# Kernel tuning notes

Hardware: AMD Instinct MI355X
Metric: run time of the kernel (lower is better)

The kernel has to match this reference:

```python
import jax, jax.numpy as jnp
import numpy as np

NUM_CLASSES = 21
TOP_K = 200
CONF_THRESH = 0.01
NMS_THRESH = 0.45
VAR0, VAR1 = 0.1, 0.2
B, P = 64, 8732  # SSD300 VOC prior count


def setup_inputs() -> dict:
    key = jax.random.key(0)
    k1, k2, k3 = jax.random.split(key, 3)
    loc = jax.random.normal(k1, (B, P, 4), dtype=jnp.float32)
    conf = jax.random.normal(k2, (B, P, NUM_CLASSES), dtype=jnp.float32)
    priors = jax.random.uniform(k3, (P, 4), dtype=jnp.float32, minval=0.02, maxval=1.0)
    return {"loc": loc, "conf": conf, "priors": priors}


def _decode(loc, priors):
    # loc, priors: [P, 4] (cx, cy, w, h) offsets -> corner boxes [P, 4]
    cxcy = priors[:, :2] + loc[:, :2] * VAR0 * priors[:, 2:]
    wh = priors[:, 2:] * jnp.exp(loc[:, 2:] * VAR1)
    x1y1 = cxcy - wh * 0.5
    x2y2 = x1y1 + wh
    return jnp.concatenate([x1y1, x2y2], axis=1)


def _iou_matrix(boxes):
    # boxes [K,4] -> pairwise IoU [K,K] with the original +1 pixel convention
    x1, y1, x2, y2 = boxes[:, 0], boxes[:, 1], boxes[:, 2], boxes[:, 3]
    area = (x2 - x1 + 1.0) * (y2 - y1 + 1.0)
    xx1 = jnp.maximum(x1[:, None], x1[None, :])
    yy1 = jnp.maximum(y1[:, None], y1[None, :])
    xx2 = jnp.minimum(x2[:, None], x2[None, :])
    yy2 = jnp.minimum(y2[:, None], y2[None, :])
    w = jnp.maximum(0.0, xx2 - xx1 + 1.0)
    h = jnp.maximum(0.0, yy2 - yy1 + 1.0)
    inter = w * h
    return inter / (area[:, None] + area[None, :] - inter)


def _nms_keep(boxes, valid):
    # boxes [K,4] sorted by descending score; greedy NMS as a fixed-length loop
    K = boxes.shape[0]
    iou = _iou_matrix(boxes)
    later = jnp.arange(K)[None, :] > jnp.arange(K)[:, None]  # strictly lower-priority

    def body(i, suppressed):
        keep_i = valid[i] & ~suppressed[i]
        return suppressed | (keep_i & (iou[i] > NMS_THRESH) & later[i])

    suppressed = jax.lax.fori_loop(0, K, body, jnp.zeros((K,), bool))
    return valid & ~suppressed


def _per_class(scores, decoded):
    # scores [P], decoded [P,4] -> [TOP_K, 7] rows (score, x1, y1, x2, y2, 0, 0)
    valid_p = scores > CONF_THRESH
    s = jnp.where(valid_p, scores, -1.0)
    top_s, idx = jax.lax.top_k(s, TOP_K)
    b = decoded[idx]                      # [K,4]
    valid = top_s > CONF_THRESH
    keep = _nms_keep(b, valid)
    rows = jnp.concatenate([top_s[:, None], b], axis=1)  # [K,5]
    order = jnp.argsort(~keep)            # stable: kept rows compacted to front
    rows = jnp.where(keep[order][:, None], rows[order], 0.0)
    return jnp.pad(rows, ((0, 0), (0, 2)))  # pad to width 7 (original leaves cols 5:7 zero)


def _per_image(loc_i, conf_i, priors):
    decoded = _decode(loc_i, priors)      # [P,4]
    # classes 1..C-1 (skip background class 0)
    cls_scores = conf_i[:, 1:].T          # [C-1, P]
    cls_out = jax.vmap(lambda s: _per_class(s, decoded))(cls_scores)  # [C-1,K,7]
    bg = jnp.zeros((1, TOP_K, 7), dtype=loc_i.dtype)
    return jnp.concatenate([bg, cls_out], axis=0)  # [C,K,7]


def _detect(loc, conf, priors):
    conf_soft = jax.nn.softmax(conf, axis=-1)  # SSD test phase applies softmax
    output = jax.vmap(_per_image, in_axes=(0, 0, None))(loc, conf_soft, priors)  # [B,C,K,7]
    flt = output.reshape(output.shape[0], -1, 7)  # [B, C*K, 7]
    score = flt[:, :, 0]
    idx = jnp.argsort(-score, axis=1)
    rank = jnp.argsort(idx, axis=1)
    mask = rank < TOP_K
    order = jnp.argsort(~mask, axis=1)    # stable: top-K rows, original positional order
    sel = jnp.take_along_axis(flt, order[:, :TOP_K, None], axis=1)  # [B,K,7]
    return sel.reshape(-1, 7)             # [B*K, 7], matching flt[rank < top_k]


def reference(loc, conf, priors):
    return _detect(loc, conf, priors)
```

## Files before the change

kernel.cpp:

```cpp
#include <hip/hip_runtime.h>
#include <stdint.h>

#define NUM_P 8732
#define NUM_B 64
#define NUM_CLS 21
#define TOPK 200
#define NMS_T 0.45f
#define CONF_T 0.01f
#define NL 35
#define NV4 2183
#define NL2 16
#define MAXCAND 4000
#define ORD_SENT 0x407FFFFFu
#define HI_BITS 0x17800u

__device__ __forceinline__ uint32_t ordf(float f) {
    uint32_t u = __float_as_uint(f);
    return (u & 0x80000000u) ? ~u : (u | 0x80000000u);
}
__device__ __forceinline__ float unordf(uint32_t v) {
    uint32_t u = (v & 0x80000000u) ? (v ^ 0x80000000u) : ~v;
    return __uint_as_float(u);
}

__global__ __launch_bounds__(256) void prep_kernel(const float* __restrict__ conf,
                                                   uint32_t* __restrict__ ct,
                                                   uint32_t* __restrict__ candCount) {
    __shared__ float tile[256 * NUM_CLS];
    const int bx = blockIdx.x;
    const int b = blockIdx.y;
    const int tid = threadIdx.x;
    if (bx == 0 && b == 0 && tid < NUM_B) candCount[tid] = 0u;
    const int p0 = bx * 256;
    const int np = min(256, NUM_P - p0);
    const int nf4 = (np * NUM_CLS) / 4;
    const float4* src = reinterpret_cast<const float4*>(conf + ((size_t)b * NUM_P + p0) * NUM_CLS);
    float4* dst = reinterpret_cast<float4*>(tile);
#pragma unroll
    for (int i = 0; i < 6; ++i) {
        int idx = tid + i * 256;
        if (idx < nf4) dst[idx] = src[idx];
    }
    __syncthreads();
    if (tid < np) {
        const int p = p0 + tid;
        const float* row = tile + tid * NUM_CLS;
        float x[NUM_CLS];
#pragma unroll
        for (int c = 0; c < NUM_CLS; ++c) x[c] = row[c];
        float m = x[0];
#pragma unroll
        for (int c = 1; c < NUM_CLS; ++c) m = fmaxf(m, x[c]);
        float e[NUM_CLS];
        float s = 0.0f;
#pragma unroll
        for (int c = 0; c < NUM_CLS; ++c) { e[c] = expf(x[c] - m); s += e[c]; }
#pragma unroll
        for (int c = 1; c < NUM_CLS; ++c) {
            float sc = e[c] / s;
            float sv = (sc > CONF_T) ? sc : -1.0f;
            ct[((size_t)(b * 20 + (c - 1))) * NUM_P + p] = ordf(sv);
        }
    }
}

__global__ __launch_bounds__(256, 5) void select_nms_kernel(const uint32_t* __restrict__ ct,
                                                            const float* __restrict__ loc,
                                                            const float* __restrict__ priors,
                                                            float* __restrict__ selS,
                                                            float* __restrict__ selX1,
                                                            float* __restrict__ selY1,
                                                            float* __restrict__ selX2,
                                                            float* __restrict__ selY2,
                                                            uint64_t* __restrict__ cands,
                                                            uint32_t* __restrict__ candCount) {
    __shared__ uint32_t hist[2048];
    __shared__ uint64_t skey[256];
    __shared__ uint32_t wtot[4];
    __shared__ uint32_t sh_d, sh_above, sh_bnd, sh_nsent;
    __shared__ int scnt;
    __shared__ int sh_run;

    const int blk = blockIdx.x;
    const int b = blk / 20;
    const int c = blk % 20;
    const int tid = threadIdx.x;
    const int lane = tid & 63;
    const int wv = tid >> 6;
    const uint32_t* col = ct + (size_t)blk * NUM_P;
    const uint4* colv = reinterpret_cast<const uint4*>(col);

#pragma unroll
    for (int i = 0; i < 8; ++i) hist[tid + i * 256] = 0;
    skey[tid] = 0;
    if (tid == 0) { scnt = 0; sh_run = 0; }
    __syncthreads();

    uint4 vv[9];
#pragma unroll
    for (int i = 0; i < 9; ++i) {
        int idx = tid + i * 256;
        vv[i] = make_uint4(ORD_SENT, ORD_SENT, ORD_SENT, ORD_SENT);
        if (idx < NV4) vv[i] = colv[idx];
    }
    int nsent = 0;
#pragma unroll
    for (int i = 0; i < 9; ++i) {
        int idx = tid + i * 256;
        if (idx < NV4) {
            uint32_t a0 = vv[i].x, a1 = vv[i].y, a2 = vv[i].z, a3 = vv[i].w;
            if (a0 == ORD_SENT) nsent++; else atomicAdd(&hist[(a0 >> 15) & 2047u], 1u);
            if (a1 == ORD_SENT) nsent++; else atomicAdd(&hist[(a1 >> 15) & 2047u], 1u);
            if (a2 == ORD_SENT) nsent++; else atomicAdd(&hist[(a2 >> 15) & 2047u], 1u);
            if (a3 == ORD_SENT) nsent++; else atomicAdd(&hist[(a3 >> 15) & 2047u], 1u);
        }
    }
    {
        int v = nsent;
#pragma unroll
        for (int off = 32; off; off >>= 1) v += __shfl_down(v, off);
        if (lane == 0) wtot[wv] = (uint32_t)v;
        __syncthreads();
        if (tid == 0) sh_nsent = wtot[0] + wtot[1] + wtot[2] + wtot[3];
        __syncthreads();
    }
    const int nreal = NUM_P - (int)sh_nsent;

    uint32_t emitThr = 0;
    bool ranked = false;
    uint32_t thrEq = 0;
    int needEq = 0;

    if (nreal >= TOPK) {
        {
            const int tbase = tid * 8;
            uint32_t ls = 0;
#pragma unroll
            for (int j = 0; j < 8; ++j) ls += hist[tbase + j];
            uint32_t v = ls;
#pragma unroll
            for (int off = 1; off < 64; off <<= 1) {
                uint32_t o2 = __shfl_down(v, off);
                if (lane + off < 64) v += o2;
            }
            if (lane == 0) wtot[wv] = v;
            __syncthreads();
            uint32_t above_wave = 0;
            for (int w = wv + 1; w < 4; ++w) above_wave += wtot[w];
            uint32_t acc = (v + above_wave) - ls;
            for (int j = 7; j >= 0; --j) {
                uint32_t h = hist[tbase + j];
                if (acc < (uint32_t)TOPK && acc + h >= (uint32_t)TOPK) {
                    sh_d = (uint32_t)(tbase + j);
                    sh_above = acc;
                    sh_bnd = h;
                }
                acc += h;
            }
            __syncthreads();
        }
        uint32_t d1 = sh_d;
        int cert = (int)sh_above;
        int need = TOPK - cert;
        int bnd = (int)sh_bnd;
        const uint32_t lvl1 = HI_BITS | d1;

        if (cert + bnd <= 256) {
            emitThr = lvl1 << 15;
        } else {
            __syncthreads();
#pragma unroll
            for (int i = 0; i < 8; ++i) hist[tid + i * 256] = 0;
            __syncthreads();
#pragma unroll
            for (int i = 0; i < 9; ++i) {
                int idx = tid + i * 256;
                if (idx < NV4) {
                    if ((vv[i].x >> 15) == lvl1) atomicAdd(&hist[(vv[i].x >> 4) & 2047u], 1u);
                    if ((vv[i].y >> 15) == lvl1) atomicAdd(&hist[(vv[i].y >> 4) & 2047u], 1u);
                    if ((vv[i].z >> 15) == lvl1) atomicAdd(&hist[(vv[i].z >> 4) & 2047u], 1u);
                    if ((vv[i].w >> 15) == lvl1) atomicAdd(&hist[(vv[i].w >> 4) & 2047u], 1u);
                }
            }
            __syncthreads();
            {
                const int tbase = tid * 8;
                uint32_t ls = 0;
#pragma unroll
                for (int j = 0; j < 8; ++j) ls += hist[tbase + j];
                uint32_t v = ls;
#pragma unroll
                for (int off = 1; off < 64; off <<= 1) {
                    uint32_t o2 = __shfl_down(v, off);
                    if (lane + off < 64) v += o2;
                }
                if (lane == 0) wtot[wv] = v;
                __syncthreads();
                uint32_t above_wave = 0;
                for (int w = wv + 1; w < 4; ++w) above_wave += wtot[w];
                uint32_t acc = (v + above_wave) - ls;
                for (int j = 7; j >= 0; --j) {
                    uint32_t h = hist[tbase + j];
                    if (acc < (uint32_t)need && acc + h >= (uint32_t)need) {
                        sh_d = (uint32_t)(tbase + j);
                        sh_above = acc;
                        sh_bnd = h;
                    }
                    acc += h;
                }
                __syncthreads();
            }
            uint32_t d2 = sh_d;
            cert += (int)sh_above;
            need -= (int)sh_above;
            bnd = (int)sh_bnd;
            const uint32_t pfx28 = (lvl1 << 11) | d2;

            if (cert + bnd <= 256) {
                emitThr = pfx28 << 4;
            } else {
                __syncthreads();
                if (tid < 16) hist[tid] = 0;
                __syncthreads();
#pragma unroll
                for (int i = 0; i < 9; ++i) {
                    int idx = tid + i * 256;
                    if (idx < NV4) {
                        if ((vv[i].x >> 4) == pfx28) atomicAdd(&hist[vv[i].x & 15u], 1u);
                        if ((vv[i].y >> 4) == pfx28) atomicAdd(&hist[vv[i].y & 15u], 1u);
                        if ((vv[i].z >> 4) == pfx28) atomicAdd(&hist[vv[i].z & 15u], 1u);
                        if ((vv[i].w >> 4) == pfx28) atomicAdd(&hist[vv[i].w & 15u], 1u);
                    }
                }
                __syncthreads();
                if (tid == 0) {
                    uint32_t acc = 0;
                    for (int j = 15; j >= 0; --j) {
                        uint32_t h = hist[j];
                        if (acc < (uint32_t)need && acc + h >= (uint32_t)need) {
                            sh_d = (uint32_t)j; sh_above = acc; sh_bnd = h; break;
                        }
                        acc += h;
                    }
                }
                __syncthreads();
                uint32_t d3 = sh_d;
                cert += (int)sh_above;
                need -= (int)sh_above;
                bnd = (int)sh_bnd;
                const uint32_t pfx32 = (pfx28 << 4) | d3;
                if (cert + bnd <= 256) {
                    emitThr = pfx32;
                } else {
                    ranked = true; thrEq = pfx32; needEq = need;
                }
            }
        }
    } else {
        ranked = true; thrEq = ORD_SENT; needEq = TOPK - nreal;
    }

    if (!ranked) {
#pragma unroll
        for (int i = 0; i < 9; ++i) {
            int idx = tid + i * 256;
            if (idx < NV4) {
                uint32_t aa[4] = {vv[i].x, vv[i].y, vv[i].z, vv[i].w};
#pragma unroll
                for (int j = 0; j < 4; ++j) {
                    uint32_t o = aa[j];
                    if (o >= emitThr) {
                        int s0 = atomicAdd(&scnt, 1);
                        uint32_t p = (uint32_t)(idx * 4 + j);
                        if (s0 < 256)
                            skey[s0] = ((uint64_t)o << 32) | (0xFFFFFFFFu - p);
                    }
                }
            }
        }
        __syncthreads();
    } else {
        for (int i = 0; i < NL; ++i) {
            int p = i * 256 + tid;
            uint32_t o = (p < NUM_P) ? col[p] : 0u;
            if (o > thrEq) {
                int s0 = atomicAdd(&scnt, 1);
                if (s0 < 256)
                    skey[s0] = ((uint64_t)o << 32) | (0xFFFFFFFFu - (uint32_t)p);
            }
            bool tie = (p < NUM_P) && (o == thrEq);
            unsigned long long ball = __ballot(tie);
            if (lane == 0) wtot[wv] = (uint32_t)__popcll(ball);
            __syncthreads();
            int rank = sh_run;
            for (int w = 0; w < wv; ++w) rank += (int)wtot[w];
            rank += __popcll(ball & ((1ull << lane) - 1ull));
            if (tie && rank < needEq) {
                int s0 = atomicAdd(&scnt, 1);
                if (s0 < 256)
                    skey[s0] = ((uint64_t)o << 32) | (0xFFFFFFFFu - (uint32_t)p);
            }
            __syncthreads();
            if (tid == 0) sh_run += (int)(wtot[0] + wtot[1] + wtot[2] + wtot[3]);
            __syncthreads();
        }
    }

    uint64_t* skey2 = reinterpret_cast<uint64_t*>(hist + 1536);
    uint64_t myk = skey[tid];
    skey2[tid] = 0;
    __syncthreads();
    int rk = 0;
#pragma unroll 8
    for (int j = 0; j < 256; ++j) rk += (skey[j] > myk) ? 1 : 0;
    if (myk != 0) skey2[rk] = myk;
    __syncthreads();

    float4* bbox4 = reinterpret_cast<float4*>(hist);
    float*  dar   = reinterpret_cast<float*>(hist) + 4 * TOPK;
    float*  dsc   = reinterpret_cast<float*>(hist) + 5 * TOPK;
    uint64_t kreg = (tid < TOPK) ? skey2[tid] : 0;
    if (tid < TOPK) {
        uint32_t p = 0xFFFFFFFFu - (uint32_t)kreg;
        float msc = unordf((uint32_t)(kreg >> 32));
        const float4 l4 = reinterpret_cast<const float4*>(loc)[(size_t)b * NUM_P + p];
        const float4 pr = reinterpret_cast<const float4*>(priors)[p];
        float cx = pr.x + (l4.x * 0.1f) * pr.z;
        float cy = pr.y + (l4.y * 0.1f) * pr.w;
        float w  = pr.z * expf(l4.z * 0.2f);
        float h  = pr.w * expf(l4.w * 0.2f);
        float mx1 = cx - w * 0.5f;
        float my1 = cy - h * 0.5f;
        float mx2 = mx1 + w;
        float my2 = my1 + h;
        bbox4[tid] = make_float4(mx1, my1, mx2, my2);
        dar[tid] = (mx2 - mx1 + 1.0f) * (my2 - my1 + 1.0f);
        dsc[tid] = msc;
    }
    __syncthreads();
    if (wv != 0) return;

    float jx1[4], jy1[4], jx2[4], jy2[4], jar[4], jsc[4];
    uint64_t validb[4], supb[4];
#pragma unroll
    for (int s = 0; s < 4; ++s) {
        int idx = s * 64 + lane;
        bool v = idx < TOPK;
        float4 bx = v ? bbox4[idx] : make_float4(0.f, 0.f, 0.f, 0.f);
        jx1[s] = bx.x; jy1[s] = bx.y; jx2[s] = bx.z; jy2[s] = bx.w;
        jar[s] = v ? dar[idx] : 1.0f;
        jsc[s] = v ? dsc[idx] : -1.0f;
        validb[s] = __ballot(v && jsc[s] > CONF_T);
        supb[s] = 0;
    }

#pragma unroll
    for (int s = 0; s < 4; ++s) {
        const int nown = (s == 3) ? (TOPK - 3 * 64) : 64;
#pragma unroll 1
        for (int o = 0; o < nown; ++o) {
            if (((validb[s] & ~supb[s]) >> o) & 1ull) {
                const int i = s * 64 + o;
                const float4 bi = bbox4[i];
                const float iar = dar[i];
#pragma unroll
                for (int s2 = s; s2 < 4; ++s2) {
                    float xx1 = fmaxf(bi.x, jx1[s2]);
                    float yy1 = fmaxf(bi.y, jy1[s2]);
                    float xx2 = fminf(bi.z, jx2[s2]);
                    float yy2 = fminf(bi.w, jy2[s2]);
                    float w = fmaxf(0.0f, xx2 - xx1 + 1.0f);
                    float h = fmaxf(0.0f, yy2 - yy1 + 1.0f);
                    float inter = w * h;
                    float iou = inter / (iar + jar[s2] - inter);
                    int idx2 = s2 * 64 + lane;
                    bool later = (s2 > s) ? (idx2 < TOPK) : (lane > o);
                    bool hit = (iou > NMS_T) && later;
                    supb[s2] |= __ballot(hit);
                }
            }
        }
    }

    const size_t base = (size_t)blk * TOPK;
    int off = 0;
    uint64_t wkey[4];
    int wrank[4];
    bool wk[4];
#pragma unroll
    for (int s = 0; s < 4; ++s) {
        uint64_t ball = validb[s] & ~supb[s];
        bool kept = (ball >> lane) & 1ull;
        int rank = off + __popcll(ball & ((1ull << lane) - 1ull));
        wk[s] = kept;
        wrank[s] = rank;
        wkey[s] = 0;
        if (kept) {
            selS[base + rank] = jsc[s];
            selX1[base + rank] = jx1[s];
            selY1[base + rank] = jy1[s];
            selX2[base + rank] = jx2[s];
            selY2[base + rank] = jy2[s];
            uint32_t pos = (uint32_t)(c + 1) * TOPK + (uint32_t)rank;
            wkey[s] = ((uint64_t)ordf(jsc[s]) << 32) | (uint32_t)(0xFFFFFFFFu - pos);
        }
        off += __popcll(ball);
    }
    uint32_t bcast = 0;
    if (lane == 0) bcast = atomicAdd(&candCount[b], (uint32_t)off);
    bcast = (uint32_t)__shfl((int)bcast, 0);
#pragma unroll
    for (int s = 0; s < 4; ++s)
        if (wk[s]) cands[(size_t)b * MAXCAND + bcast + wrank[s]] = wkey[s];
}

__global__ __launch_bounds__(256) void final_kernel(const uint64_t* __restrict__ cands,
                                                    const uint32_t* __restrict__ candCount,
                                                    const float* __restrict__ selS,
                                                    const float* __restrict__ selX1,
                                                    const float* __restrict__ selY1,
                                                    const float* __restrict__ selX2,
                                                    const float* __restrict__ selY2,
                                                    float* __restrict__ out) {
    __shared__ uint32_t hist[2048];
    __shared__ uint64_t skey[256];
    __shared__ uint32_t posArr[TOPK];
    __shared__ uint32_t sortedPos[TOPK];
    __shared__ uint32_t wtot[4];
    __shared__ int wsum[2][4];
    __shared__ uint32_t sh_d, sh_above, sh_bnd;
    __shared__ int scnt;

    const int b = blockIdx.x;
    const int tid = threadIdx.x;
    const int lane = tid & 63;
    const int wv = tid >> 6;
    const int n = (int)candCount[b];

    uint64_t key[NL2];
#pragma unroll
    for (int i = 0; i < NL2; ++i) {
        int idx = tid + i * 256;
        key[i] = (idx < n) ? cands[(size_t)b * MAXCAND + idx] : 0ull;
    }
#pragma unroll
    for (int i = 0; i < 8; ++i) hist[tid + i * 256] = 0;
    skey[tid] = 0;
    if (tid == 0) scnt = 0;
    __syncthreads();

    uint64_t emitThr = 1;
    if (n > TOPK) {
#pragma unroll
        for (int i = 0; i < NL2; ++i)
            if (key[i] != 0ull) atomicAdd(&hist[(uint32_t)(key[i] >> 47) & 2047u], 1u);
        __syncthreads();
        {
            const int tbase = tid * 8;
            uint32_t ls = 0;
#pragma unroll
            for (int j = 0; j < 8; ++j) ls += hist[tbase + j];
            uint32_t v = ls;
#pragma unroll
            for (int off = 1; off < 64; off <<= 1) {
                uint32_t o2 = __shfl_down(v, off);
                if (lane + off < 64) v += o2;
            }
            if (lane == 0) wtot[wv] = v;
            __syncthreads();
            uint32_t above_wave = 0;
            for (int w = wv + 1; w < 4; ++w) above_wave += wtot[w];
            uint32_t acc = (v + above_wave) - ls;
            for (int j = 7; j >= 0; --j) {
                uint32_t h = hist[tbase + j];
                if (acc < (uint32_t)TOPK && acc + h >= (uint32_t)TOPK) {
                    sh_d = (uint32_t)(tbase + j);
                    sh_above = acc;
                    sh_bnd = h;
                }
                acc += h;
            }
            __syncthreads();
        }
        if (sh_above + sh_bnd <= 256u) {
            emitThr = (uint64_t)(HI_BITS | sh_d) << 47;
        } else {
            uint64_t prefix = 0;
            for (int bit = 63; bit >= 0; --bit) {
                uint64_t cand = prefix | (1ull << bit);
                int cnt = 0;
#pragma unroll
                for (int i = 0; i < NL2; ++i) cnt += (key[i] >= cand) ? 1 : 0;
                for (int off = 32; off; off >>= 1) cnt += __shfl_down(cnt, off);
                int bufi = bit & 1;
                if (lane == 0) wsum[bufi][wv] = cnt;
                __syncthreads();
                int tot = wsum[bufi][0] + wsum[bufi][1] + wsum[bufi][2] + wsum[bufi][3];
                if (tot >= TOPK) prefix = cand;
            }
            emitThr = prefix;
        }
    }

#pragma unroll
    for (int i = 0; i < NL2; ++i) {
        if (key[i] != 0ull && key[i] >= emitThr) {
            int s0 = atomicAdd(&scnt, 1);
            if (s0 < 256) skey[s0] = key[i];
        }
    }
    __syncthreads();
    const int nsel = min(scnt, TOPK);

    uint64_t myk = skey[tid];
    __syncthreads();
    int rk = 0;
#pragma unroll 8
    for (int j = 0; j < 256; ++j) rk += (skey[j] > myk) ? 1 : 0;
    if (myk != 0 && rk < TOPK) posArr[rk] = 0xFFFFFFFFu - (uint32_t)myk;
    __syncthreads();

    if (tid < nsel) {
        uint32_t mypos = posArr[tid];
        int pr = 0;
        for (int j = 0; j < nsel; ++j) pr += (posArr[j] < mypos) ? 1 : 0;
        sortedPos[pr] = mypos;
    }
    __syncthreads();

    if (tid < TOPK) {
        int T = TOPK - nsel;
        float* o = out + ((size_t)b * TOPK + tid) * 7;
        if (tid < T) {
            o[0] = 0.f; o[1] = 0.f; o[2] = 0.f; o[3] = 0.f; o[4] = 0.f; o[5] = 0.f; o[6] = 0.f;
        } else {
            uint32_t pos = sortedPos[tid - T];
            uint32_t cc = pos / TOPK;
            uint32_t sl = pos % TOPK;
            size_t r = ((size_t)b * 20 + (cc - 1)) * TOPK + sl;
            o[0] = selS[r]; o[1] = selX1[r]; o[2] = selY1[r]; o[3] = selX2[r]; o[4] = selY2[r];
            o[5] = 0.f; o[6] = 0.f;
        }
    }
}

extern "C" void kernel_launch(void* const* d_in, const int* in_sizes, int n_in,
                              void* d_out, int out_size, void* d_ws, size_t ws_size,
                              hipStream_t stream) {
    const float* loc    = (const float*)d_in[0];
    const float* conf   = (const float*)d_in[1];
    const float* priors = (const float*)d_in[2];
    float* out = (float*)d_out;

    const size_t CAND_BYTES = (size_t)NUM_B * MAXCAND * sizeof(uint64_t);
    const size_t SEL_ONE    = (size_t)NUM_B * 20 * TOPK * sizeof(float);
    const size_t CNT_BYTES  = 256;

    char* ws = (char*)d_ws;
    uint64_t* cands     = (uint64_t*)ws;
    float*    selS      = (float*)(ws + CAND_BYTES);
    float*    selX1     = (float*)(ws + CAND_BYTES + SEL_ONE);
    float*    selY1     = (float*)(ws + CAND_BYTES + 2 * SEL_ONE);
    float*    selX2     = (float*)(ws + CAND_BYTES + 3 * SEL_ONE);
    float*    selY2     = (float*)(ws + CAND_BYTES + 4 * SEL_ONE);
    uint32_t* candCount = (uint32_t*)(ws + CAND_BYTES + 5 * SEL_ONE);
    uint32_t* ct        = (uint32_t*)(ws + CAND_BYTES + 5 * SEL_ONE + CNT_BYTES);

    dim3 pgrid(35, NUM_B);
    prep_kernel<<<pgrid, 256, 0, stream>>>(conf, ct, candCount);
    select_nms_kernel<<<NUM_B * 20, 256, 0, stream>>>(ct, loc, priors,
                                                      selS, selX1, selY1, selX2, selY2,
                                                      cands, candCount);
    final_kernel<<<NUM_B, 256, 0, stream>>>(cands, candCount,
                                            selS, selX1, selY1, selX2, selY2, out);
}
```

Before: 63.73 us.

## Compress class-score columns to 16-bit keys and recompute exact scores for selected candidates

The prep kernel now writes a 16-bit truncated order-preserving key per prior and class, padded to an aligned pitch, plus the per-prior softmax max and sum, in place of full 32-bit keys. The select kernel builds its histograms on the 16-bit keys, keeps candidate prior indices, resolves ties at the threshold bucket by recomputing exact softmax scores from conf, and rebuilds the 64-bit sort keys only for the selected entries. This halves the intermediate score traffic and cuts the number of radix refinement passes. In exchange it adds a denominator buffer, scattered conf reloads for the selected candidates, and a more complex tie-handling path.

```diff
diff --git a/kernel.cpp b/kernel.cpp
--- a/kernel.cpp
+++ b/kernel.cpp
@@ -7,8 +7,8 @@
 #define TOPK 200
 #define NMS_T 0.45f
 #define CONF_T 0.01f
-#define NL 35
-#define NV4 2183
+#define PITCH16 8736
+#define NV8 1092
 #define NL2 16
 #define MAXCAND 4000
 #define ORD_SENT 0x407FFFFFu
@@ -24,7 +24,8 @@
 }
 
 __global__ __launch_bounds__(256) void prep_kernel(const float* __restrict__ conf,
-                                                   uint32_t* __restrict__ ct,
+                                                   uint16_t* __restrict__ ct16,
+                                                   float2* __restrict__ denom,
                                                    uint32_t* __restrict__ candCount) {
     __shared__ float tile[256 * NUM_CLS];
     const int bx = blockIdx.x;
@@ -55,16 +56,24 @@
         float s = 0.0f;
 #pragma unroll
         for (int c = 0; c < NUM_CLS; ++c) { e[c] = expf(x[c] - m); s += e[c]; }
+        denom[(size_t)b * NUM_P + p] = make_float2(m, s);
 #pragma unroll
         for (int c = 1; c < NUM_CLS; ++c) {
             float sc = e[c] / s;
-            float sv = (sc > CONF_T) ? sc : -1.0f;
-            ct[((size_t)(b * 20 + (c - 1))) * NUM_P + p] = ordf(sv);
-        }
+            uint16_t u = 0;
+            if (sc > CONF_T) u = (uint16_t)((ordf(sc) >> 10) & 0xFFFFu);
+            ct16[((size_t)(b * 20 + (c - 1))) * PITCH16 + p] = u;
+        }
+    } else if (p0 + tid >= NUM_P && p0 + tid < PITCH16) {
+#pragma unroll
+        for (int c = 1; c < NUM_CLS; ++c)
+            ct16[((size_t)(b * 20 + (c - 1))) * PITCH16 + (p0 + tid)] = 0;
     }
 }
 
-__global__ __launch_bounds__(256, 5) void select_nms_kernel(const uint32_t* __restrict__ ct,
+__global__ __launch_bounds__(256, 5) void select_nms_kernel(const uint16_t* __restrict__ ct16,
+                                                            const float* __restrict__ conf,
+                                                            const float2* __restrict__ denom,
                                                             const float* __restrict__ loc,
                                                             const float* __restrict__ priors,
                                                             float* __restrict__ selS,
@@ -76,8 +85,9 @@
                                                             uint32_t* __restrict__ candCount) {
     __shared__ uint32_t hist[2048];
     __shared__ uint64_t skey[256];
+    __shared__ uint32_t plist[256];
     __shared__ uint32_t wtot[4];
-    __shared__ uint32_t sh_d, sh_above, sh_bnd, sh_nsent;
+    __shared__ uint32_t sh_d, sh_above, sh_bnd, sh_nsent, sh_tcnt;
     __shared__ int scnt;
     __shared__ int sh_run;
 
@@ -87,32 +97,34 @@
     const int tid = threadIdx.x;
     const int lane = tid & 63;
     const int wv = tid >> 6;
-    const uint32_t* col = ct + (size_t)blk * NUM_P;
-    const uint4* colv = reinterpret_cast<const uint4*>(col);
+    const uint4* colv = reinterpret_cast<const uint4*>(ct16 + (size_t)blk * PITCH16);
+    const size_t ibase = (size_t)b * NUM_P;
 
 #pragma unroll
     for (int i = 0; i < 8; ++i) hist[tid + i * 256] = 0;
     skey[tid] = 0;
-    if (tid == 0) { scnt = 0; sh_run = 0; }
-    __syncthreads();
-
-    uint4 vv[9];
-#pragma unroll
-    for (int i = 0; i < 9; ++i) {
+    if (tid == 0) { scnt = 0; sh_run = 0; sh_tcnt = 0; }
+    __syncthreads();
+
+    uint4 uu[5];
+#pragma unroll
+    for (int i = 0; i < 5; ++i) {
         int idx = tid + i * 256;
-        vv[i] = make_uint4(ORD_SENT, ORD_SENT, ORD_SENT, ORD_SENT);
-        if (idx < NV4) vv[i] = colv[idx];
+        uu[i] = make_uint4(0, 0, 0, 0);
+        if (idx < NV8) uu[i] = colv[idx];
     }
     int nsent = 0;
 #pragma unroll
-    for (int i = 0; i < 9; ++i) {
+    for (int i = 0; i < 5; ++i) {
         int idx = tid + i * 256;
-        if (idx < NV4) {
-            uint32_t a0 = vv[i].x, a1 = vv[i].y, a2 = vv[i].z, a3 = vv[i].w;
-            if (a0 == ORD_SENT) nsent++; else atomicAdd(&hist[(a0 >> 15) & 2047u], 1u);
-            if (a1 == ORD_SENT) nsent++; else atomicAdd(&hist[(a1 >> 15) & 2047u], 1u);
-            if (a2 == ORD_SENT) nsent++; else atomicAdd(&hist[(a2 >> 15) & 2047u], 1u);
-            if (a3 == ORD_SENT) nsent++; else atomicAdd(&hist[(a3 >> 15) & 2047u], 1u);
+        if (idx < NV8) {
+            uint32_t ww[4] = {uu[i].x, uu[i].y, uu[i].z, uu[i].w};
+#pragma unroll
+            for (int q = 0; q < 4; ++q) {
+                uint32_t lo = ww[q] & 0xFFFFu, hi = ww[q] >> 16;
+                if (lo) atomicAdd(&hist[lo >> 5], 1u); else nsent++;
+                if (hi) atomicAdd(&hist[hi >> 5], 1u); else nsent++;
+            }
         }
     }
     {
@@ -124,12 +136,11 @@
         if (tid == 0) sh_nsent = wtot[0] + wtot[1] + wtot[2] + wtot[3];
         __syncthreads();
     }
-    const int nreal = NUM_P - (int)sh_nsent;
-
-    uint32_t emitThr = 0;
-    bool ranked = false;
-    uint32_t thrEq = 0;
-    int needEq = 0;
+    const int nreal = PITCH16 - (int)sh_nsent;
+
+    int mode;
+    uint32_t thr16 = 1;
+    int need3 = 0, needEq = 0;
 
     if (nreal >= TOPK) {
         {
@@ -161,150 +172,198 @@
         }
         uint32_t d1 = sh_d;
         int cert = (int)sh_above;
-        int need = TOPK - cert;
         int bnd = (int)sh_bnd;
-        const uint32_t lvl1 = HI_BITS | d1;
 
         if (cert + bnd <= 256) {
-            emitThr = lvl1 << 15;
+            thr16 = d1 << 5;
+            mode = 0;
         } else {
             __syncthreads();
-#pragma unroll
-            for (int i = 0; i < 8; ++i) hist[tid + i * 256] = 0;
-            __syncthreads();
-#pragma unroll
-            for (int i = 0; i < 9; ++i) {
+            if (tid < 32) hist[tid] = 0;
+            __syncthreads();
+#pragma unroll
+            for (int i = 0; i < 5; ++i) {
                 int idx = tid + i * 256;
-                if (idx < NV4) {
-                    if ((vv[i].x >> 15) == lvl1) atomicAdd(&hist[(vv[i].x >> 4) & 2047u], 1u);
-                    if ((vv[i].y >> 15) == lvl1) atomicAdd(&hist[(vv[i].y >> 4) & 2047u], 1u);
-                    if ((vv[i].z >> 15) == lvl1) atomicAdd(&hist[(vv[i].z >> 4) & 2047u], 1u);
-                    if ((vv[i].w >> 15) == lvl1) atomicAdd(&hist[(vv[i].w >> 4) & 2047u], 1u);
-                }
-            }
-            __syncthreads();
-            {
-                const int tbase = tid * 8;
-                uint32_t ls = 0;
-#pragma unroll
-                for (int j = 0; j < 8; ++j) ls += hist[tbase + j];
-                uint32_t v = ls;
-#pragma unroll
-                for (int off = 1; off < 64; off <<= 1) {
-                    uint32_t o2 = __shfl_down(v, off);
-                    if (lane + off < 64) v += o2;
-                }
-                if (lane == 0) wtot[wv] = v;
-                __syncthreads();
-                uint32_t above_wave = 0;
-                for (int w = wv + 1; w < 4; ++w) above_wave += wtot[w];
-                uint32_t acc = (v + above_wave) - ls;
-                for (int j = 7; j >= 0; --j) {
-                    uint32_t h = hist[tbase + j];
+                if (idx < NV8) {
+                    uint32_t ww[4] = {uu[i].x, uu[i].y, uu[i].z, uu[i].w};
+#pragma unroll
+                    for (int q = 0; q < 4; ++q) {
+                        uint32_t lo = ww[q] & 0xFFFFu, hi = ww[q] >> 16;
+                        if ((lo >> 5) == d1) atomicAdd(&hist[lo & 31u], 1u);
+                        if ((hi >> 5) == d1) atomicAdd(&hist[hi & 31u], 1u);
+                    }
+                }
+            }
+            __syncthreads();
+            const int need = TOPK - cert;
+            if (tid == 0) {
+                uint32_t acc = 0;
+                for (int j = 31; j >= 0; --j) {
+                    uint32_t h = hist[j];
                     if (acc < (uint32_t)need && acc + h >= (uint32_t)need) {
-                        sh_d = (uint32_t)(tbase + j);
-                        sh_above = acc;
-                        sh_bnd = h;
+                        sh_d = (uint32_t)j; sh_above = acc; sh_bnd = h; break;
                     }
                     acc += h;
                 }
-                __syncthreads();
-            }
-            uint32_t d2 = sh_d;
+            }
+            __syncthreads();
             cert += (int)sh_above;
-            need -= (int)sh_above;
             bnd = (int)sh_bnd;
-            const uint32_t pfx28 = (lvl1 << 11) | d2;
-
+            thr16 = (d1 << 5) | sh_d;
             if (cert + bnd <= 256) {
-                emitThr = pfx28 << 4;
+                mode = 0;
             } else {
-                __syncthreads();
-                if (tid < 16) hist[tid] = 0;
-                __syncthreads();
-#pragma unroll
-                for (int i = 0; i < 9; ++i) {
-                    int idx = tid + i * 256;
-                    if (idx < NV4) {
-                        if ((vv[i].x >> 4) == pfx28) atomicAdd(&hist[vv[i].x & 15u], 1u);
-                        if ((vv[i].y >> 4) == pfx28) atomicAdd(&hist[vv[i].y & 15u], 1u);
-                        if ((vv[i].z >> 4) == pfx28) atomicAdd(&hist[vv[i].z & 15u], 1u);
-                        if ((vv[i].w >> 4) == pfx28) atomicAdd(&hist[vv[i].w & 15u], 1u);
+                mode = 1;
+                need3 = TOPK - cert;
+            }
+        }
+    } else {
+        mode = 2;
+        thr16 = 1;
+        needEq = TOPK - nreal;
+    }
+
+    const uint32_t emitLo = (mode == 1) ? thr16 + 1 : thr16;
+#pragma unroll
+    for (int i = 0; i < 5; ++i) {
+        int idx = tid + i * 256;
+        if (idx < NV8) {
+            uint32_t ww[4] = {uu[i].x, uu[i].y, uu[i].z, uu[i].w};
+#pragma unroll
+            for (int q = 0; q < 4; ++q) {
+                uint32_t lo = ww[q] & 0xFFFFu, hi = ww[q] >> 16;
+                if (lo >= emitLo) {
+                    int s0 = atomicAdd(&scnt, 1);
+                    if (s0 < 256) plist[s0] = (uint32_t)(idx * 8 + q * 2);
+                }
+                if (hi >= emitLo) {
+                    int s0 = atomicAdd(&scnt, 1);
+                    if (s0 < 256) plist[s0] = (uint32_t)(idx * 8 + q * 2 + 1);
+                }
+            }
+        }
+    }
+    __syncthreads();
+
+    if (mode == 1) {
+#pragma unroll
+        for (int i = 0; i < 5; ++i) {
+            int idx = tid + i * 256;
+            if (idx < NV8) {
+                uint32_t ww[4] = {uu[i].x, uu[i].y, uu[i].z, uu[i].w};
+#pragma unroll
+                for (int q = 0; q < 4; ++q) {
+                    uint32_t lo = ww[q] & 0xFFFFu, hi = ww[q] >> 16;
+                    if (lo == thr16) {
+                        uint32_t t = atomicAdd(&sh_tcnt, 1u);
+                        if (t < 1024u) hist[t] = (uint32_t)(idx * 8 + q * 2);
                     }
-                }
-                __syncthreads();
-                if (tid == 0) {
-                    uint32_t acc = 0;
-                    for (int j = 15; j >= 0; --j) {
-                        uint32_t h = hist[j];
-                        if (acc < (uint32_t)need && acc + h >= (uint32_t)need) {
-                            sh_d = (uint32_t)j; sh_above = acc; sh_bnd = h; break;
-                        }
-                        acc += h;
+                    if (hi == thr16) {
+                        uint32_t t = atomicAdd(&sh_tcnt, 1u);
+                        if (t < 1024u) hist[t] = (uint32_t)(idx * 8 + q * 2 + 1);
                     }
                 }
-                __syncthreads();
-                uint32_t d3 = sh_d;
-                cert += (int)sh_above;
-                need -= (int)sh_above;
-                bnd = (int)sh_bnd;
-                const uint32_t pfx32 = (pfx28 << 4) | d3;
-                if (cert + bnd <= 256) {
-                    emitThr = pfx32;
-                } else {
-                    ranked = true; thrEq = pfx32; needEq = need;
-                }
-            }
-        }
-    } else {
-        ranked = true; thrEq = ORD_SENT; needEq = TOPK - nreal;
-    }
-
-    if (!ranked) {
-#pragma unroll
-        for (int i = 0; i < 9; ++i) {
+            }
+        }
+        __syncthreads();
+        const int tn = min((int)sh_tcnt, 1024);
+        uint32_t myp[4];
+#pragma unroll
+        for (int s = 0; s < 4; ++s) {
+            int t = tid + s * 256;
+            myp[s] = (t < tn) ? hist[t] : 0xFFFFFFFFu;
+        }
+        __syncthreads();
+        uint64_t* tkey = reinterpret_cast<uint64_t*>(hist);
+        uint64_t myk4[4];
+#pragma unroll
+        for (int s = 0; s < 4; ++s) {
+            int t = tid + s * 256;
+            myk4[s] = 0;
+            if (t < tn) {
+                uint32_t p = myp[s];
+                float x = conf[(ibase + p) * NUM_CLS + (c + 1)];
+                float2 ms = denom[ibase + p];
+                float sc = expf(x - ms.x) / ms.y;
+                uint64_t k = ((uint64_t)ordf(sc) << 32) | (0xFFFFFFFFu - p);
+                tkey[t] = k;
+                myk4[s] = k;
+            }
+        }
+        __syncthreads();
+#pragma unroll
+        for (int s = 0; s < 4; ++s) {
+            int t = tid + s * 256;
+            if (t < tn) {
+                uint64_t k = myk4[s];
+                int r = 0;
+                for (int j = 0; j < tn; ++j) r += (tkey[j] > k) ? 1 : 0;
+                if (r < need3) {
+                    int s0 = atomicAdd(&scnt, 1);
+                    if (s0 < 256) plist[s0] = 0xFFFFFFFFu - (uint32_t)k;
+                }
+            }
+        }
+        __syncthreads();
+    } else if (mode == 2) {
+        for (int i = 0; i < 5; ++i) {
             int idx = tid + i * 256;
-            if (idx < NV4) {
-                uint32_t aa[4] = {vv[i].x, vv[i].y, vv[i].z, vv[i].w};
-#pragma unroll
-                for (int j = 0; j < 4; ++j) {
-                    uint32_t o = aa[j];
-                    if (o >= emitThr) {
+            uint32_t flags = 0;
+            int lc = 0;
+            if (idx < NV8) {
+                uint32_t ww[4] = {uu[i].x, uu[i].y, uu[i].z, uu[i].w};
+#pragma unroll
+                for (int q = 0; q < 4; ++q) {
+                    uint32_t lo = ww[q] & 0xFFFFu, hi = ww[q] >> 16;
+                    int p0 = idx * 8 + q * 2;
+                    if (lo == 0 && p0 < NUM_P) { flags |= 1u << (q * 2); lc++; }
+                    if (hi == 0 && p0 + 1 < NUM_P) { flags |= 1u << (q * 2 + 1); lc++; }
+                }
+            }
+            uint32_t v = (uint32_t)lc;
+#pragma unroll
+            for (int off = 1; off < 64; off <<= 1) {
+                uint32_t o2 = __shfl_up(v, off);
+                if (lane >= off) v += o2;
+            }
+            if (lane == 63) wtot[wv] = v;
+            __syncthreads();
+            int woff = sh_run;
+            for (int w = 0; w < wv; ++w) woff += (int)wtot[w];
+            int base = woff + (int)v - lc;
+            int r = 0;
+#pragma unroll
+            for (int j = 0; j < 8; ++j) {
+                if ((flags >> j) & 1u) {
+                    if (base + r < needEq) {
                         int s0 = atomicAdd(&scnt, 1);
-                        uint32_t p = (uint32_t)(idx * 4 + j);
-                        if (s0 < 256)
-                            skey[s0] = ((uint64_t)o << 32) | (0xFFFFFFFFu - p);
+                        if (s0 < 256) plist[s0] = (uint32_t)(idx * 8 + j) | 0x80000000u;
                     }
-                }
-            }
-        }
-        __syncthreads();
-    } else {
-        for (int i = 0; i < NL; ++i) {
-            int p = i * 256 + tid;
-            uint32_t o = (p < NUM_P) ? col[p] : 0u;
-            if (o > thrEq) {
-                int s0 = atomicAdd(&scnt, 1);
-                if (s0 < 256)
-                    skey[s0] = ((uint64_t)o << 32) | (0xFFFFFFFFu - (uint32_t)p);
-            }
-            bool tie = (p < NUM_P) && (o == thrEq);
-            unsigned long long ball = __ballot(tie);
-            if (lane == 0) wtot[wv] = (uint32_t)__popcll(ball);
-            __syncthreads();
-            int rank = sh_run;
-            for (int w = 0; w < wv; ++w) rank += (int)wtot[w];
-            rank += __popcll(ball & ((1ull << lane) - 1ull));
-            if (tie && rank < needEq) {
-                int s0 = atomicAdd(&scnt, 1);
-                if (s0 < 256)
-                    skey[s0] = ((uint64_t)o << 32) | (0xFFFFFFFFu - (uint32_t)p);
+                    r++;
+                }
             }
             __syncthreads();
             if (tid == 0) sh_run += (int)(wtot[0] + wtot[1] + wtot[2] + wtot[3]);
             __syncthreads();
         }
     }
+
+    const int nsel = min(scnt, 256);
+    if (tid < nsel) {
+        uint32_t e = plist[tid];
+        uint32_t p = e & 0x7FFFFFFFu;
+        uint32_t o;
+        if (e & 0x80000000u) {
+            o = ORD_SENT;
+        } else {
+            float x = conf[(ibase + p) * NUM_CLS + (c + 1)];
+            float2 ms = denom[ibase + p];
+            float sc = expf(x - ms.x) / ms.y;
+            o = ordf(sc);
+        }
+        skey[tid] = ((uint64_t)o << 32) | (0xFFFFFFFFu - p);
+    }
+    __syncthreads();
 
     uint64_t* skey2 = reinterpret_cast<uint64_t*>(hist + 1536);
     uint64_t myk = skey[tid];
@@ -323,7 +382,7 @@
     if (tid < TOPK) {
         uint32_t p = 0xFFFFFFFFu - (uint32_t)kreg;
         float msc = unordf((uint32_t)(kreg >> 32));
-        const float4 l4 = reinterpret_cast<const float4*>(loc)[(size_t)b * NUM_P + p];
+        const float4 l4 = reinterpret_cast<const float4*>(loc)[ibase + p];
         const float4 pr = reinterpret_cast<const float4*>(priors)[p];
         float cx = pr.x + (l4.x * 0.1f) * pr.z;
         float cy = pr.y + (l4.y * 0.1f) * pr.w;
@@ -552,9 +611,10 @@
     const float* priors = (const float*)d_in[2];
     float* out = (float*)d_out;
 
-    const size_t CAND_BYTES = (size_t)NUM_B * MAXCAND * sizeof(uint64_t);
-    const size_t SEL_ONE    = (size_t)NUM_B * 20 * TOPK * sizeof(float);
-    const size_t CNT_BYTES  = 256;
+    const size_t CAND_BYTES  = (size_t)NUM_B * MAXCAND * sizeof(uint64_t);
+    const size_t SEL_ONE     = (size_t)NUM_B * 20 * TOPK * sizeof(float);
+    const size_t CNT_BYTES   = 256;
+    const size_t DENOM_BYTES = (size_t)NUM_B * NUM_P * sizeof(float2);
 
     char* ws = (char*)d_ws;
     uint64_t* cands     = (uint64_t*)ws;
@@ -564,11 +624,12 @@
     float*    selX2     = (float*)(ws + CAND_BYTES + 3 * SEL_ONE);
     float*    selY2     = (float*)(ws + CAND_BYTES + 4 * SEL_ONE);
     uint32_t* candCount = (uint32_t*)(ws + CAND_BYTES + 5 * SEL_ONE);
-    uint32_t* ct        = (uint32_t*)(ws + CAND_BYTES + 5 * SEL_ONE + CNT_BYTES);
+    float2*   denom     = (float2*)(ws + CAND_BYTES + 5 * SEL_ONE + CNT_BYTES);
+    uint16_t* ct16      = (uint16_t*)(ws + CAND_BYTES + 5 * SEL_ONE + CNT_BYTES + DENOM_BYTES);
 
     dim3 pgrid(35, NUM_B);
-    prep_kernel<<<pgrid, 256, 0, stream>>>(conf, ct, candCount);
-    select_nms_kernel<<<NUM_B * 20, 256, 0, stream>>>(ct, loc, priors,
+    prep_kernel<<<pgrid, 256, 0, stream>>>(conf, ct16, denom, candCount);
+    select_nms_kernel<<<NUM_B * 20, 256, 0, stream>>>(ct16, conf, denom, loc, priors,
                                                       selS, selX1, selY1, selX2, selY2,
                                                       cands, candCount);
     final_kernel<<<NUM_B, 256, 0, stream>>>(cands, candCount,
```

Result: slower. 66.89 us (+5.0%).
